# Kernel optimization log

Measured on AMD Instinct MI355X. Metric: run time of the kernel, lower is better.

Reference implementation:

```python
import jax, jax.numpy as jnp
import numpy as np
from functools import partial

N = 512
H, W = 324, 332
C = 120
NEAR, FAR, BG = 0.01, 100.0, 1.0


def setup_inputs() -> dict:
    key = jax.random.key(0)
    k1, k2, k3, k4, k5, k6 = jax.random.split(key, 6)
    # positions: small xy, depth z in [2, 8] so everything projects on screen
    xy = 0.5 * jax.random.normal(k1, (N, 2), dtype=jnp.float32)
    z = jax.random.uniform(k2, (N, 1), dtype=jnp.float32, minval=2.0, maxval=8.0)
    positions = jnp.concatenate([xy, z], axis=-1)  # [N,3]
    rotations = jax.random.normal(k3, (N, 4), dtype=jnp.float32)  # unused by the math
    # scales in [0.5, 4.5] pixels -> small footprints, early-break never triggers
    scales = jax.random.uniform(k4, (N, 3), dtype=jnp.float32) * 4.0 + 0.5
    opacities = jax.random.uniform(k5, (N,), dtype=jnp.float32)
    spectral_features = jax.random.uniform(k6, (N, C), dtype=jnp.float32)
    tone_mapping = jnp.ones((C,), dtype=jnp.float32)
    intrinsics = jnp.array([[300.0, 0.0, 166.0],
                            [0.0, 300.0, 162.0],
                            [0.0, 0.0, 1.0]], dtype=jnp.float32)
    extrinsics = jnp.eye(4, dtype=jnp.float32)
    return {"positions": positions, "rotations": rotations, "scales": scales,
            "opacities": opacities, "spectral_features": spectral_features,
            "tone_mapping": tone_mapping, "intrinsics": intrinsics,
            "extrinsics": extrinsics}


def _render(positions, scales, opacities, spectral_features, tone_mapping,
            intrinsics, extrinsics):
    # --- projection (world -> camera -> screen) ---
    ph = jnp.concatenate([positions, jnp.ones_like(positions[:, :1])], axis=-1)  # [N,4]
    cam = ph @ extrinsics.T                     # [N,4]
    cam3 = cam[:, :3]
    proj = cam3 @ intrinsics.T                  # [N,3]
    screen = proj[:, :2] / (proj[:, 2:3] + 1e-6)  # [N,2] (x, y)
    depths = cam3[:, 2]                         # [N]

    # --- frustum / screen culling mask (kept as a validity flag) ---
    valid = (depths > NEAR) & (depths < FAR)
    valid &= (screen[:, 0] > -100.0) & (screen[:, 0] < W + 100.0)
    valid &= (screen[:, 1] > -100.0) & (screen[:, 1] < H + 100.0)

    # --- 2D covariance: diag(scale_x^2, scale_y^2), regularized inverse ---
    s2 = scales[:, :2] ** 2
    cov = jnp.zeros((positions.shape[0], 2, 2), dtype=positions.dtype)
    cov = cov.at[:, 0, 0].set(s2[:, 0]).at[:, 1, 1].set(s2[:, 1])
    cov_inv = jnp.linalg.inv(cov + 1e-4 * jnp.eye(2, dtype=positions.dtype))  # [N,2,2]

    # --- depth sort (front to back) ---
    order = jnp.argsort(depths)
    screen_s = screen[order]
    depths_s = depths[order]
    cinv_s = cov_inv[order]
    op_s = opacities[order]
    valid_s = valid[order]
    spec_s = spectral_features[order]           # [N,C]

    # pixel grid: pix[h,w] = (x=w, y=h)
    X, Y = jnp.meshgrid(jnp.arange(W), jnp.arange(H))  # each [H,W]
    pix = jnp.stack([X, Y], axis=-1).astype(positions.dtype)  # [H,W,2]

    def step(A, g):
        pos, cinv, op, v = g
        done = jnp.mean(A) > 0.99  # torch early-break condition
        off = (pos[0] < -W) | (pos[0] > 2 * W) | (pos[1] < -H) | (pos[1] > 2 * H)
        skip = done | off | jnp.logical_not(v)
        diff = pix - pos                                    # [H,W,2]
        mahal = jnp.einsum('hwi,ij,hwj->hw', diff, cinv, diff)
        alpha = op * jnp.exp(-0.5 * mahal) * (1.0 - A)      # [H,W]
        alpha = jnp.where(skip, 0.0, alpha)
        return A + alpha, alpha

    A0 = jnp.zeros((H, W), dtype=positions.dtype)
    A_final, alphas = jax.lax.scan(step, A0, (screen_s, cinv_s, op_s, valid_s))  # alphas [N,H,W]

    # spectral/depth accumulation == sum_i feature_i * alpha_i (GEMM over N)
    spectral = jnp.einsum('nc,nhw->chw', spec_s, alphas)    # [C,H,W]
    depth_img = jnp.einsum('n,nhw->hw', depths_s, alphas)   # [H,W]
    spectral = spectral + BG * (1.0 - A_final)[None]
    spectral = spectral * tone_mapping[:, None, None]
    return spectral, depth_img, A_final


def reference(positions, rotations, scales, opacities, spectral_features,
              tone_mapping, intrinsics, extrinsics):
    # rotations are accepted but unused by the original math (diagonal 2D cov)
    return _render(positions, scales, opacities, spectral_features,
                   tone_mapping, intrinsics, extrinsics)
```

## Files before the change

kernel.cpp:

```cpp
#include <hip/hip_runtime.h>
#include <math.h>

#define N_G 512
#define IMG_H 324
#define IMG_W 332
#define N_C 120
#define HW (IMG_H*IMG_W)
#define TSX 21
#define TSY 81
#define NT (TSX*TSY)
#define NBLK (NT*4)


__global__ __launch_bounds__(256, 6) void k_render(
    const float* __restrict__ pos, const float* __restrict__ scales,
    const float* __restrict__ opac, const float* __restrict__ Km,
    const float* __restrict__ Em, const float* __restrict__ spec,
    const float* __restrict__ tm, float* __restrict__ out)
{
  __shared__ float prm[N_G*8];
  __shared__ float key[N_G+4];
  __shared__ int wcnt[4];

  const int tid  = threadIdx.x;
  const int w    = tid >> 6;
  const int lane = tid & 63;
  const int tx = lane & 15, ty = lane >> 4;
  const unsigned long long ltm = (1ull << lane) - 1ull;

  const int t  = blockIdx.x >> 2;
  const int cq = blockIdx.x & 3;

  float psx[2], psy[2], pc00[2], pc11[2], pl2[2], pd[2];
  float bxmin[2], bxmax[2], bymin[2], bymax[2];
  {
    const float E0=Em[0],E1=Em[1],E2=Em[2],E3=Em[3],
                E4=Em[4],E5=Em[5],E6=Em[6],E7=Em[7],
                E8=Em[8],E9=Em[9],E10=Em[10],E11=Em[11];
    const float K0=Km[0],K1=Km[1],K2=Km[2],
                K3=Km[3],K4=Km[4],K5=Km[5],
                K6=Km[6],K7=Km[7],K8=Km[8];
    #pragma unroll
    for (int q = 0; q < 2; ++q) {
      const int g = w*128 + lane + q*64;
      float p0 = pos[g*3+0], p1 = pos[g*3+1], p2 = pos[g*3+2];
      float cam0 = E0*p0 + E1*p1 + E2*p2  + E3;
      float cam1 = E4*p0 + E5*p1 + E6*p2  + E7;
      float cam2 = E8*p0 + E9*p1 + E10*p2 + E11;
      float pr0 = K0*cam0 + K1*cam1 + K2*cam2;
      float pr1 = K3*cam0 + K4*cam1 + K5*cam2;
      float pr2 = K6*cam0 + K7*cam1 + K8*cam2;
      float inv = 1.0f/(pr2 + 1e-6f);
      float sx = pr0*inv, sy = pr1*inv;
      float depth = cam2;
      bool valid = (depth > 0.01f) && (depth < 100.0f)
                && (sx > -100.0f) && (sx < (float)IMG_W + 100.0f)
                && (sy > -100.0f) && (sy < (float)IMG_H + 100.0f);
      bool off = (sx < -(float)IMG_W) || (sx > 2.0f*(float)IMG_W)
              || (sy < -(float)IMG_H) || (sy > 2.0f*(float)IMG_H);
      bool skip = off || (!valid);
      float s0 = scales[g*3+0], s1 = scales[g*3+1];
      float v0 = s0*s0 + 1e-4f, v1 = s1*s1 + 1e-4f;
      const float HL2E = 0.72134752f;
      psx[q] = sx; psy[q] = sy;
      pc00[q] = HL2E/v0; pc11[q] = HL2E/v1;
      pl2[q] = __log2f(skip ? 0.0f : opac[g]);
      pd[q]  = depth;
      float rx = 6.0f*sqrtf(v0);
      float ry = 6.0f*sqrtf(v1);
      bxmin[q] = skip ?  1e9f : sx - rx;
      bxmax[q] = skip ? -1e9f : sx + rx;
      bymin[q] = skip ?  1e9f : sy - ry;
      bymax[q] = skip ? -1e9f : sy + ry;
    }
  }

  const int jx = t % TSX, ky = t / TSX;
  const int bx = 10 + ((jx & 1) ? ((jx+1)>>1) : -((jx+1)>>1));
  const int by = 40 + ((ky & 1) ? ((ky+1)>>1) : -((ky+1)>>1));

  const int x = bx*16 + tx;
  const int y = by*4 + ty;
  const bool inb = (x < IMG_W) && (y < IMG_H);
  const float px = (float)min(x, IMG_W-1);
  const float py = (float)min(y, IMG_H-1);
  const float wxmin = (float)(bx*16), wxmax = wxmin + 15.0f;
  const float wymin = (float)(by*4),  wymax = wymin + 3.0f;

  bool h0 = !(bxmin[0] > wxmax || bxmax[0] < wxmin ||
              bymin[0] > wymax || bymax[0] < wymin);
  bool h1 = !(bxmin[1] > wxmax || bxmax[1] < wxmin ||
              bymin[1] > wymax || bymax[1] < wymin);
  unsigned long long m0 = __ballot(h0), m1 = __ballot(h1);
  int c0 = __popcll(m0);
  if (lane == 0) wcnt[w] = c0 + __popcll(m1);
  __syncthreads();
  int offw = 0;
  #pragma unroll
  for (int k = 0; k < 4; ++k) if (k < w) offw += wcnt[k];
  const int nh = wcnt[0] + wcnt[1] + wcnt[2] + wcnt[3];
  const int p0 = offw + __popcll(m0 & ltm);
  const int p1 = offw + c0 + __popcll(m1 & ltm);
  if (h0) key[p0] = pd[0];
  if (h1) key[p1] = pd[1];
  if (tid < 4) key[nh + tid] = 1e30f;
  __syncthreads();

  if (h0 | h1) {
    int r0 = 0, r1 = 0;
    const float d0 = pd[0], d1 = pd[1];
    for (int j = 0; j < nh; j += 4) {
      float4 k4 = *(const float4*)&key[j];
      if (h0) {
        r0 += (k4.x < d0 || (k4.x == d0 && j+0 < p0)) ? 1 : 0;
        r0 += (k4.y < d0 || (k4.y == d0 && j+1 < p0)) ? 1 : 0;
        r0 += (k4.z < d0 || (k4.z == d0 && j+2 < p0)) ? 1 : 0;
        r0 += (k4.w < d0 || (k4.w == d0 && j+3 < p0)) ? 1 : 0;
      }
      if (h1) {
        r1 += (k4.x < d1 || (k4.x == d1 && j+0 < p1)) ? 1 : 0;
        r1 += (k4.y < d1 || (k4.y == d1 && j+1 < p1)) ? 1 : 0;
        r1 += (k4.z < d1 || (k4.z == d1 && j+2 < p1)) ? 1 : 0;
        r1 += (k4.w < d1 || (k4.w == d1 && j+3 < p1)) ? 1 : 0;
      }
    }
    if (h0) {
      *(float4*)&prm[r0*8]   = make_float4(psx[0], psy[0], pc00[0], pc11[0]);
      *(float4*)&prm[r0*8+4] = make_float4(pl2[0], pd[0],
                                 __int_as_float((w*128 + lane)*N_C), 0.0f);
    }
    if (h1) {
      *(float4*)&prm[r1*8]   = make_float4(psx[1], psy[1], pc00[1], pc11[1]);
      *(float4*)&prm[r1*8+4] = make_float4(pl2[1], pd[1],
                                 __int_as_float((w*128 + lane + 64)*N_C), 0.0f);
    }
  }
  __syncthreads();

  float T = 1.0f, dacc = 0.0f;
  float4 acc0 = {0,0,0,0}, acc1 = {0,0,0,0};
  const int g0 = cq + 8*w;
  const bool g1ok = (g0 + 4) < 30;
  const float* specg0 = spec + 4*g0;

  #pragma unroll 2
  for (int j = 0; j < nh; ++j) {
    float4 q0 = *(const float4*)&prm[j*8];
    float4 q1 = *(const float4*)&prm[j*8+4];
    float dx = px - q0.x, dy = py - q0.y;
    float e = q1.x - (q0.z*dx*dx + q0.w*dy*dy);
    if (__ballot(e > -30.0f)) {
      float a  = exp2f(e);
      float wv = a * T;
      T *= (1.0f - a);
      if (cq == 2) dacc = fmaf(q1.y, wv, dacc);
      const int sbase = __float_as_int(q1.z);
      float4 s0 = *(const float4*)(specg0 + sbase);
      acc0.x = fmaf(wv, s0.x, acc0.x);
      acc0.y = fmaf(wv, s0.y, acc0.y);
      acc0.z = fmaf(wv, s0.z, acc0.z);
      acc0.w = fmaf(wv, s0.w, acc0.w);
      if (g1ok) {
        float4 s1 = *(const float4*)(specg0 + sbase + 16);
        acc1.x = fmaf(wv, s1.x, acc1.x);
        acc1.y = fmaf(wv, s1.y, acc1.y);
        acc1.z = fmaf(wv, s1.z, acc1.z);
        acc1.w = fmaf(wv, s1.w, acc1.w);
      }
      if (!__ballot(T >= 1e-5f)) break;
    }
  }

  if (inb) {
    const int pixi = y*IMG_W + x;
    const float bgT = T;
    float4 t0 = *(const float4*)&tm[4*g0];
    out[(4*g0+0)*HW + pixi] = (acc0.x + bgT)*t0.x;
    out[(4*g0+1)*HW + pixi] = (acc0.y + bgT)*t0.y;
    out[(4*g0+2)*HW + pixi] = (acc0.z + bgT)*t0.z;
    out[(4*g0+3)*HW + pixi] = (acc0.w + bgT)*t0.w;
    if (g1ok) {
      const int g1 = g0 + 4;
      float4 t1 = *(const float4*)&tm[4*g1];
      out[(4*g1+0)*HW + pixi] = (acc1.x + bgT)*t1.x;
      out[(4*g1+1)*HW + pixi] = (acc1.y + bgT)*t1.y;
      out[(4*g1+2)*HW + pixi] = (acc1.z + bgT)*t1.z;
      out[(4*g1+3)*HW + pixi] = (acc1.w + bgT)*t1.w;
    }
    if (cq == 2 && w == 0) out[N_C*HW + pixi] = dacc;
    if (cq == 3 && w == 0) out[N_C*HW + HW + pixi] = 1.0f - T;
  }
}

extern "C" void kernel_launch(void* const* d_in, const int* in_sizes, int n_in,
                              void* d_out, int out_size, void* d_ws, size_t ws_size,
                              hipStream_t stream) {
  const float* pos    = (const float*)d_in[0];
  const float* scales = (const float*)d_in[2];
  const float* opac   = (const float*)d_in[3];
  const float* spec   = (const float*)d_in[4];
  const float* tm     = (const float*)d_in[5];
  const float* K      = (const float*)d_in[6];
  const float* E      = (const float*)d_in[7];
  float* out = (float*)d_out;
  (void)d_ws; (void)ws_size;

  k_render<<<NBLK, 256, 0, stream>>>(pos, scales, opac, K, E, spec, tm, out);
}
```

Before: 122.9 us.

## Merge channel-quarter blocks into one 512-thread block sharing alpha evaluation

Each tile was previously handled by four 256-thread blocks, each covering a quarter of the channels, and every block redid the projection, binning, depth sort and Gaussian alpha evaluation. Now a single 512-thread block per tile has 8 waves that each handle a 4-channel group at strides of 32. The waves cooperatively compute alphas in chunks of 64 Gaussians into shared memory, along with a live mask. This removes the fourfold duplication of preprocessing, sorting and exp work, at the cost of extra per-chunk barriers, coarser early termination, more shared memory and fewer blocks.

New measurement: 124.0 us. Within noise of the previous version (+0.9%).

```diff
diff --git a/kernel.cpp b/kernel.cpp
--- a/kernel.cpp
+++ b/kernel.cpp
@@ -6,21 +6,23 @@
 #define IMG_W 332
 #define N_C 120
 #define HW (IMG_H*IMG_W)
+#define CHUNK 64
 #define TSX 21
 #define TSY 81
 #define NT (TSX*TSY)
-#define NBLK (NT*4)
-
-
-__global__ __launch_bounds__(256, 6) void k_render(
+
+
+__global__ __launch_bounds__(512, 6) void k_render(
     const float* __restrict__ pos, const float* __restrict__ scales,
     const float* __restrict__ opac, const float* __restrict__ Km,
     const float* __restrict__ Em, const float* __restrict__ spec,
     const float* __restrict__ tm, float* __restrict__ out)
 {
-  __shared__ float prm[N_G*8];
-  __shared__ float key[N_G+4];
-  __shared__ int wcnt[4];
+  __shared__ __align__(16) float prm[N_G*8];
+  __shared__ __align__(16) float buf[CHUNK*64];
+  __shared__ __align__(16) float key[N_G+4];
+  __shared__ unsigned long long livem[8];
+  __shared__ int wcnt[8];
 
   const int tid  = threadIdx.x;
   const int w    = tid >> 6;
@@ -28,11 +30,8 @@
   const int tx = lane & 15, ty = lane >> 4;
   const unsigned long long ltm = (1ull << lane) - 1ull;
 
-  const int t  = blockIdx.x >> 2;
-  const int cq = blockIdx.x & 3;
-
-  float psx[2], psy[2], pc00[2], pc11[2], pl2[2], pd[2];
-  float bxmin[2], bxmax[2], bymin[2], bymax[2];
+  float psx, psy, pc00, pc11, pl2, pdep;
+  float bxmin, bxmax, bymin, bymax;
   {
     const float E0=Em[0],E1=Em[1],E2=Em[2],E3=Em[3],
                 E4=Em[4],E5=Em[5],E6=Em[6],E7=Em[7],
@@ -40,41 +39,39 @@
     const float K0=Km[0],K1=Km[1],K2=Km[2],
                 K3=Km[3],K4=Km[4],K5=Km[5],
                 K6=Km[6],K7=Km[7],K8=Km[8];
-    #pragma unroll
-    for (int q = 0; q < 2; ++q) {
-      const int g = w*128 + lane + q*64;
-      float p0 = pos[g*3+0], p1 = pos[g*3+1], p2 = pos[g*3+2];
-      float cam0 = E0*p0 + E1*p1 + E2*p2  + E3;
-      float cam1 = E4*p0 + E5*p1 + E6*p2  + E7;
-      float cam2 = E8*p0 + E9*p1 + E10*p2 + E11;
-      float pr0 = K0*cam0 + K1*cam1 + K2*cam2;
-      float pr1 = K3*cam0 + K4*cam1 + K5*cam2;
-      float pr2 = K6*cam0 + K7*cam1 + K8*cam2;
-      float inv = 1.0f/(pr2 + 1e-6f);
-      float sx = pr0*inv, sy = pr1*inv;
-      float depth = cam2;
-      bool valid = (depth > 0.01f) && (depth < 100.0f)
-                && (sx > -100.0f) && (sx < (float)IMG_W + 100.0f)
-                && (sy > -100.0f) && (sy < (float)IMG_H + 100.0f);
-      bool off = (sx < -(float)IMG_W) || (sx > 2.0f*(float)IMG_W)
-              || (sy < -(float)IMG_H) || (sy > 2.0f*(float)IMG_H);
-      bool skip = off || (!valid);
-      float s0 = scales[g*3+0], s1 = scales[g*3+1];
-      float v0 = s0*s0 + 1e-4f, v1 = s1*s1 + 1e-4f;
-      const float HL2E = 0.72134752f;
-      psx[q] = sx; psy[q] = sy;
-      pc00[q] = HL2E/v0; pc11[q] = HL2E/v1;
-      pl2[q] = __log2f(skip ? 0.0f : opac[g]);
-      pd[q]  = depth;
-      float rx = 6.0f*sqrtf(v0);
-      float ry = 6.0f*sqrtf(v1);
-      bxmin[q] = skip ?  1e9f : sx - rx;
-      bxmax[q] = skip ? -1e9f : sx + rx;
-      bymin[q] = skip ?  1e9f : sy - ry;
-      bymax[q] = skip ? -1e9f : sy + ry;
-    }
-  }
-
+    const int g = tid;
+    float p0 = pos[g*3+0], p1 = pos[g*3+1], p2 = pos[g*3+2];
+    float cam0 = E0*p0 + E1*p1 + E2*p2  + E3;
+    float cam1 = E4*p0 + E5*p1 + E6*p2  + E7;
+    float cam2 = E8*p0 + E9*p1 + E10*p2 + E11;
+    float pr0 = K0*cam0 + K1*cam1 + K2*cam2;
+    float pr1 = K3*cam0 + K4*cam1 + K5*cam2;
+    float pr2 = K6*cam0 + K7*cam1 + K8*cam2;
+    float inv = 1.0f/(pr2 + 1e-6f);
+    float sx = pr0*inv, sy = pr1*inv;
+    float depth = cam2;
+    bool valid = (depth > 0.01f) && (depth < 100.0f)
+              && (sx > -100.0f) && (sx < (float)IMG_W + 100.0f)
+              && (sy > -100.0f) && (sy < (float)IMG_H + 100.0f);
+    bool off = (sx < -(float)IMG_W) || (sx > 2.0f*(float)IMG_W)
+            || (sy < -(float)IMG_H) || (sy > 2.0f*(float)IMG_H);
+    bool skip = off || (!valid);
+    float s0 = scales[g*3+0], s1 = scales[g*3+1];
+    float v0 = s0*s0 + 1e-4f, v1 = s1*s1 + 1e-4f;
+    const float HL2E = 0.72134752f;
+    psx = sx; psy = sy;
+    pc00 = HL2E/v0; pc11 = HL2E/v1;
+    pl2 = __log2f(skip ? 0.0f : opac[g]);
+    pdep = depth;
+    float rx = 6.0f*sqrtf(v0);
+    float ry = 6.0f*sqrtf(v1);
+    bxmin = skip ?  1e9f : sx - rx;
+    bxmax = skip ? -1e9f : sx + rx;
+    bymin = skip ?  1e9f : sy - ry;
+    bymax = skip ? -1e9f : sy + ry;
+  }
+
+  const int t = blockIdx.x;
   const int jx = t % TSX, ky = t / TSX;
   const int bx = 10 + ((jx & 1) ? ((jx+1)>>1) : -((jx+1)>>1));
   const int by = 40 + ((ky & 1) ? ((ky+1)>>1) : -((ky+1)>>1));
@@ -87,108 +84,114 @@
   const float wxmin = (float)(bx*16), wxmax = wxmin + 15.0f;
   const float wymin = (float)(by*4),  wymax = wymin + 3.0f;
 
-  bool h0 = !(bxmin[0] > wxmax || bxmax[0] < wxmin ||
-              bymin[0] > wymax || bymax[0] < wymin);
-  bool h1 = !(bxmin[1] > wxmax || bxmax[1] < wxmin ||
-              bymin[1] > wymax || bymax[1] < wymin);
-  unsigned long long m0 = __ballot(h0), m1 = __ballot(h1);
-  int c0 = __popcll(m0);
-  if (lane == 0) wcnt[w] = c0 + __popcll(m1);
+  bool hit = !(bxmin > wxmax || bxmax < wxmin ||
+               bymin > wymax || bymax < wymin);
+  unsigned long long m = __ballot(hit);
+  if (lane == 0) wcnt[w] = __popcll(m);
   __syncthreads();
   int offw = 0;
   #pragma unroll
-  for (int k = 0; k < 4; ++k) if (k < w) offw += wcnt[k];
-  const int nh = wcnt[0] + wcnt[1] + wcnt[2] + wcnt[3];
-  const int p0 = offw + __popcll(m0 & ltm);
-  const int p1 = offw + c0 + __popcll(m1 & ltm);
-  if (h0) key[p0] = pd[0];
-  if (h1) key[p1] = pd[1];
+  for (int k = 0; k < 8; ++k) if (k < w) offw += wcnt[k];
+  int nh = 0;
+  #pragma unroll
+  for (int k = 0; k < 8; ++k) nh += wcnt[k];
+  const int p = offw + __popcll(m & ltm);
+  if (hit) key[p] = pdep;
   if (tid < 4) key[nh + tid] = 1e30f;
   __syncthreads();
 
-  if (h0 | h1) {
-    int r0 = 0, r1 = 0;
-    const float d0 = pd[0], d1 = pd[1];
+  if (hit) {
+    int r = 0;
+    const float d = pdep;
     for (int j = 0; j < nh; j += 4) {
       float4 k4 = *(const float4*)&key[j];
-      if (h0) {
-        r0 += (k4.x < d0 || (k4.x == d0 && j+0 < p0)) ? 1 : 0;
-        r0 += (k4.y < d0 || (k4.y == d0 && j+1 < p0)) ? 1 : 0;
-        r0 += (k4.z < d0 || (k4.z == d0 && j+2 < p0)) ? 1 : 0;
-        r0 += (k4.w < d0 || (k4.w == d0 && j+3 < p0)) ? 1 : 0;
-      }
-      if (h1) {
-        r1 += (k4.x < d1 || (k4.x == d1 && j+0 < p1)) ? 1 : 0;
-        r1 += (k4.y < d1 || (k4.y == d1 && j+1 < p1)) ? 1 : 0;
-        r1 += (k4.z < d1 || (k4.z == d1 && j+2 < p1)) ? 1 : 0;
-        r1 += (k4.w < d1 || (k4.w == d1 && j+3 < p1)) ? 1 : 0;
-      }
-    }
-    if (h0) {
-      *(float4*)&prm[r0*8]   = make_float4(psx[0], psy[0], pc00[0], pc11[0]);
-      *(float4*)&prm[r0*8+4] = make_float4(pl2[0], pd[0],
-                                 __int_as_float((w*128 + lane)*N_C), 0.0f);
-    }
-    if (h1) {
-      *(float4*)&prm[r1*8]   = make_float4(psx[1], psy[1], pc00[1], pc11[1]);
-      *(float4*)&prm[r1*8+4] = make_float4(pl2[1], pd[1],
-                                 __int_as_float((w*128 + lane + 64)*N_C), 0.0f);
-    }
+      r += (k4.x < d || (k4.x == d && j+0 < p)) ? 1 : 0;
+      r += (k4.y < d || (k4.y == d && j+1 < p)) ? 1 : 0;
+      r += (k4.z < d || (k4.z == d && j+2 < p)) ? 1 : 0;
+      r += (k4.w < d || (k4.w == d && j+3 < p)) ? 1 : 0;
+    }
+    *(float4*)&prm[r*8]   = make_float4(psx, psy, pc00, pc11);
+    *(float4*)&prm[r*8+4] = make_float4(pl2, pdep,
+                               __int_as_float(tid*N_C), 0.0f);
   }
   __syncthreads();
 
   float T = 1.0f, dacc = 0.0f;
-  float4 acc0 = {0,0,0,0}, acc1 = {0,0,0,0};
-  const int g0 = cq + 8*w;
-  const bool g1ok = (g0 + 4) < 30;
-  const float* specg0 = spec + 4*g0;
-
-  #pragma unroll 2
-  for (int j = 0; j < nh; ++j) {
-    float4 q0 = *(const float4*)&prm[j*8];
-    float4 q1 = *(const float4*)&prm[j*8+4];
-    float dx = px - q0.x, dy = py - q0.y;
-    float e = q1.x - (q0.z*dx*dx + q0.w*dy*dy);
-    if (__ballot(e > -30.0f)) {
-      float a  = exp2f(e);
+  float4 acc0={0,0,0,0}, acc1={0,0,0,0}, acc2={0,0,0,0}, acc3={0,0,0,0};
+  const int gch = 4*w;
+  const bool g3ok = (w < 6);
+
+  for (int cb = 0; cb < nh; cb += CHUNK) {
+    const int nc = min(CHUNK, nh - cb);
+
+    unsigned long long lm = 0;
+    #pragma unroll 2
+    for (int j = w; j < nc; j += 8) {
+      float4 q0 = *(const float4*)&prm[(cb+j)*8];
+      float l2op = prm[(cb+j)*8+4];
+      float dx = px - q0.x, dy = py - q0.y;
+      float e = l2op - (q0.z*dx*dx + q0.w*dy*dy);
+      buf[j*64 + lane] = exp2f(e);
+      if (__ballot(e > -30.0f)) lm |= 1ull << j;
+    }
+    if (lane == 0) livem[w] = lm;
+    __syncthreads();
+    unsigned long long mm = livem[0]|livem[1]|livem[2]|livem[3]
+                           |livem[4]|livem[5]|livem[6]|livem[7];
+
+    #pragma unroll 2
+    for (int j = 0; mm; ++j, mm >>= 1) {
+      if (!(mm & 1ull)) continue;
+      float a = buf[j*64 + lane];
+      float4 q1 = *(const float4*)&prm[(cb+j)*8+4];
       float wv = a * T;
       T *= (1.0f - a);
-      if (cq == 2) dacc = fmaf(q1.y, wv, dacc);
-      const int sbase = __float_as_int(q1.z);
-      float4 s0 = *(const float4*)(specg0 + sbase);
+      if (w == 0) dacc = fmaf(q1.y, wv, dacc);
+      const float* sp = spec + __float_as_int(q1.z) + gch;
+      float4 s0 = *(const float4*)(sp);
+      float4 s1 = *(const float4*)(sp + 32);
+      float4 s2 = *(const float4*)(sp + 64);
       acc0.x = fmaf(wv, s0.x, acc0.x);
       acc0.y = fmaf(wv, s0.y, acc0.y);
       acc0.z = fmaf(wv, s0.z, acc0.z);
       acc0.w = fmaf(wv, s0.w, acc0.w);
-      if (g1ok) {
-        float4 s1 = *(const float4*)(specg0 + sbase + 16);
-        acc1.x = fmaf(wv, s1.x, acc1.x);
-        acc1.y = fmaf(wv, s1.y, acc1.y);
-        acc1.z = fmaf(wv, s1.z, acc1.z);
-        acc1.w = fmaf(wv, s1.w, acc1.w);
+      acc1.x = fmaf(wv, s1.x, acc1.x);
+      acc1.y = fmaf(wv, s1.y, acc1.y);
+      acc1.z = fmaf(wv, s1.z, acc1.z);
+      acc1.w = fmaf(wv, s1.w, acc1.w);
+      acc2.x = fmaf(wv, s2.x, acc2.x);
+      acc2.y = fmaf(wv, s2.y, acc2.y);
+      acc2.z = fmaf(wv, s2.z, acc2.z);
+      acc2.w = fmaf(wv, s2.w, acc2.w);
+      if (g3ok) {
+        float4 s3 = *(const float4*)(sp + 96);
+        acc3.x = fmaf(wv, s3.x, acc3.x);
+        acc3.y = fmaf(wv, s3.y, acc3.y);
+        acc3.z = fmaf(wv, s3.z, acc3.z);
+        acc3.w = fmaf(wv, s3.w, acc3.w);
       }
-      if (!__ballot(T >= 1e-5f)) break;
-    }
+    }
+    __syncthreads();
+    if (!__ballot(T >= 1e-5f)) break;
   }
 
   if (inb) {
     const int pixi = y*IMG_W + x;
     const float bgT = T;
-    float4 t0 = *(const float4*)&tm[4*g0];
-    out[(4*g0+0)*HW + pixi] = (acc0.x + bgT)*t0.x;
-    out[(4*g0+1)*HW + pixi] = (acc0.y + bgT)*t0.y;
-    out[(4*g0+2)*HW + pixi] = (acc0.z + bgT)*t0.z;
-    out[(4*g0+3)*HW + pixi] = (acc0.w + bgT)*t0.w;
-    if (g1ok) {
-      const int g1 = g0 + 4;
-      float4 t1 = *(const float4*)&tm[4*g1];
-      out[(4*g1+0)*HW + pixi] = (acc1.x + bgT)*t1.x;
-      out[(4*g1+1)*HW + pixi] = (acc1.y + bgT)*t1.y;
-      out[(4*g1+2)*HW + pixi] = (acc1.z + bgT)*t1.z;
-      out[(4*g1+3)*HW + pixi] = (acc1.w + bgT)*t1.w;
-    }
-    if (cq == 2 && w == 0) out[N_C*HW + pixi] = dacc;
-    if (cq == 3 && w == 0) out[N_C*HW + HW + pixi] = 1.0f - T;
+    #pragma unroll
+    for (int k = 0; k < 4; ++k) {
+      const int c = gch + 32*k;
+      if (c < N_C) {
+        float4 a4 = (k==0) ? acc0 : (k==1) ? acc1 : (k==2) ? acc2 : acc3;
+        float4 t4 = *(const float4*)&tm[c];
+        out[(c+0)*HW + pixi] = (a4.x + bgT)*t4.x;
+        out[(c+1)*HW + pixi] = (a4.y + bgT)*t4.y;
+        out[(c+2)*HW + pixi] = (a4.z + bgT)*t4.z;
+        out[(c+3)*HW + pixi] = (a4.w + bgT)*t4.w;
+      }
+    }
+    if (w == 0) out[N_C*HW + pixi] = dacc;
+    if (w == 1) out[N_C*HW + HW + pixi] = 1.0f - T;
   }
 }
 
@@ -205,5 +208,5 @@
   float* out = (float*)d_out;
   (void)d_ws; (void)ws_size;
 
-  k_render<<<NBLK, 256, 0, stream>>>(pos, scales, opac, K, E, spec, tm, out);
+  k_render<<<NT, 512, 0, stream>>>(pos, scales, opac, K, E, spec, tm, out);
 }
```
